# Kernel optimization log

Measured on AMD Instinct MI355X. Metric: run time of the kernel, lower is better.

The kernel has to match this reference:

```python
import jax, jax.numpy as jnp
import numpy as np

NEG = -9e15
LN_EPS = 1e-5
ALPHA = 0.2  # LeakyReLU negative slope


def setup_inputs() -> dict:
    key = jax.random.key(0)
    ks = jax.random.split(key, 10)
    B, N, Din, H, F, L = 8, 512, 64, 8, 128, 2
    x = jax.random.normal(ks[0], (B, N, Din), dtype=jnp.float32)
    adj = jax.random.randint(ks[1], (B, N, N), 0, 2, dtype=jnp.int32)
    Wp = jax.random.normal(ks[2], (Din, F), dtype=jnp.float32) * 0.12
    bp = jnp.zeros((F,), dtype=jnp.float32)
    W_heads = jax.random.normal(ks[3], (L, H, F, F), dtype=jnp.float32) * 0.08
    a_heads = jax.random.normal(ks[4], (L, H, 2 * F), dtype=jnp.float32) * 0.08
    W_out = jax.random.normal(ks[5], (L, H * F, F), dtype=jnp.float32) * 0.03
    a_out = jax.random.normal(ks[6], (L, 2 * F), dtype=jnp.float32) * 0.08
    ln_g = jnp.ones((L, F), dtype=jnp.float32)
    ln_b = jnp.zeros((L, F), dtype=jnp.float32)
    return {"x": x, "adj": adj, "Wp": Wp, "bp": bp, "W_heads": W_heads,
            "a_heads": a_heads, "W_out": W_out, "a_out": a_out,
            "ln_g": ln_g, "ln_b": ln_b}


def _gat_heads(x, W, a, adj_mask):
    # x:[B,N,Fin]  W:[H,Fin,F]  a:[H,2F]  adj_mask:[B,N,N] bool
    h = jnp.einsum('bni,hio->bhno', x, W)          # [B,H,N,F]
    F = h.shape[-1]
    # a_input @ a == (h_i . a1) + (h_j . a2): split attention vector,
    # mathematically identical to the concat formulation.
    s1 = jnp.einsum('bhnf,hf->bhn', h, a[:, :F])   # source term
    s2 = jnp.einsum('bhnf,hf->bhn', h, a[:, F:])   # target term
    e = jax.nn.leaky_relu(s1[:, :, :, None] + s2[:, :, None, :], ALPHA)  # [B,H,N,N]
    att = jnp.where(adj_mask[:, None], e, NEG)
    att = jax.nn.softmax(att, axis=-1)
    return jnp.einsum('bhnm,bhmf->bhnf', att, h)   # [B,H,N,F]


def _gat_single(x, W, a, adj_mask):
    # out_att head (concat=False, no ELU)
    h = jnp.einsum('bni,io->bno', x, W)            # [B,N,F]
    F = h.shape[-1]
    s1 = h @ a[:F]                                  # [B,N]
    s2 = h @ a[F:]
    e = jax.nn.leaky_relu(s1[:, :, None] + s2[:, None, :], ALPHA)
    att = jnp.where(adj_mask, e, NEG)
    att = jax.nn.softmax(att, axis=-1)
    return jnp.einsum('bnm,bmf->bnf', att, h)


def _layernorm(x, g, b):
    mu = jnp.mean(x, axis=-1, keepdims=True)
    var = jnp.var(x, axis=-1, keepdims=True)
    return (x - mu) * jax.lax.rsqrt(var + LN_EPS) * g + b


def reference(x, adj, Wp, bp, W_heads, a_heads, W_out, a_out, ln_g, ln_b):
    adj_mask = adj > 0                              # [B,N,N]
    L = W_heads.shape[0]
    B, N = x.shape[0], x.shape[1]
    # input projection (eval mode -> dropout is identity)
    h = jax.nn.relu(x @ Wp + bp)                    # [B,N,F]
    for i in range(L):
        residual = h
        heads = _gat_heads(h, W_heads[i], a_heads[i], adj_mask)      # [B,H,N,F]
        heads = jax.nn.elu(heads)                                     # concat=True -> ELU
        multi = jnp.transpose(heads, (0, 2, 1, 3)).reshape(B, N, -1)  # [B,N,H*F]
        out = _gat_single(multi, W_out[i], a_out[i], adj_mask)        # [B,N,F]
        h = _layernorm(out + residual, ln_g[i], ln_b[i])
        if i < L - 1:
            h = jax.nn.relu(h)
    return h
```

## Files before the change

### kernel.cpp

```cpp
#include <hip/hip_runtime.h>
#include <hip/hip_cooperative_groups.h>


namespace cg = cooperative_groups;

constexpr int B = 8, N = 512, DIN = 64, H = 8, F = 128;
constexpr int BN = B * N;
constexpr float ALPHA_LR = 0.2f;
constexpr float EPS_LN = 1e-5f;
constexpr float FLOW = -3.0e38f;

typedef __attribute__((ext_vector_type(8))) short short8;
typedef __attribute__((ext_vector_type(4))) float f32x4;

__device__ __forceinline__ f32x4 mfma16(short8 a, short8 b, f32x4 c) {
  return __builtin_amdgcn_mfma_f32_16x16x32_bf16(a, b, c, 0, 0, 0);
}

__device__ __forceinline__ short f2bf(float f) {
  union { float f; unsigned u; } v;
  v.f = f;
  unsigned r = v.u + 0x7FFFu + ((v.u >> 16) & 1u);
  return (short)(r >> 16);
}

struct KParams {
  const float* x; const int* adj; const float* Wp; const float* bp;
  const float* W_heads; const float* a_heads; const float* W_out;
  const float* a_out; const float* ln_g; const float* ln_b;
  float* h; short* hb; unsigned long long* amask; short* WTh; short* WoT;
  short* hhT; short* multi; short* hsT; float* sA; float* dout;
};

struct SM_PH { short As[64 * 136]; short Bs[128 * 136]; };
struct SM_AH {
  short Vs[128 * 136]; short Pf[16 * 64 * 8]; float s2all[512];
  float s1r[64]; float mrow[64]; float linv[64]; float red[64][4];
};
struct SM_PO { short As[32 * 136]; short Bs[32 * 136]; };
struct SM_AS {
  short Vs[128 * 136]; short Pf[4 * 64 * 8]; float s2all[512];
  float Ot[16][132]; float redS[16][16]; float redQ[16][16];
  float s1r[16]; float mrow[16]; float linv[16]; float muA[16]; float rsA[16];
};
struct SM_SU { float T[32][33]; float xr[2][64]; };

__device__ __forceinline__ void st_setup(const KParams& P, int bid, int tid,
                                         char* smraw) {
  for (int i = tid; i < 288; i += 256) P.sA[(size_t)bid * 288 + i] = 0.f;
  {
    int lane = tid & 63, wv = tid >> 6;
    int v[16];
#pragma unroll
    for (int j = 0; j < 16; j++) {
      int w = (bid + j * 512) * 4 + wv;
      v[j] = P.adj[(size_t)w * 64 + lane];
    }
#pragma unroll
    for (int j = 0; j < 16; j++) {
      int w = (bid + j * 512) * 4 + wv;
      unsigned long long m = __ballot(v[j] > 0);
      if (lane == 0) P.amask[w] = m;
    }
  }
  {
    SM_SU* s = (SM_SU*)smraw;
    int half = tid >> 7, f = tid & 127;
    for (int u = bid; u < 2048; u += 512) {
      int row = u * 2 + half;
      __syncthreads();
      if (f < 64) s->xr[half][f] = P.x[(size_t)row * DIN + f];
      __syncthreads();
      float acc = P.bp[f];
#pragma unroll
      for (int i = 0; i < DIN; i++)
        acc = fmaf(s->xr[half][i], P.Wp[i * F + f], acc);
      acc = fmaxf(acc, 0.f);
      P.h[(size_t)row * F + f] = acc;
      P.hb[(size_t)row * F + f] = f2bf(acc);
    }
  }
  {
    SM_SU* s = (SM_SU*)smraw;
    const float* in; short* out; int R, C, bx, by, bt;
    if (bid < 256) {
      in = P.W_heads; out = P.WTh; R = 128; C = 128;
      bx = bid & 3; by = (bid >> 2) & 3; bt = bid >> 4;
    } else {
      int i = bid - 256;
      in = P.W_out; out = P.WoT; R = 1024; C = 128;
      bx = i & 3; by = (i >> 2) & 31; bt = i >> 7;
    }
    int c0 = bx * 32, r0 = by * 32;
    const float* ip = in + (size_t)bt * R * C;
    short* op = out + (size_t)bt * R * C;
    __syncthreads();
    {
      int r = tid >> 3, c4 = (tid & 7) * 4;
      float4 v = *(const float4*)(ip + (size_t)(r0 + r) * C + c0 + c4);
      s->T[r][c4] = v.x; s->T[r][c4 + 1] = v.y;
      s->T[r][c4 + 2] = v.z; s->T[r][c4 + 3] = v.w;
    }
    __syncthreads();
    {
      int cr = tid >> 3, q = (tid & 7) * 4;
      short4 o;
      o.x = f2bf(s->T[q][cr]); o.y = f2bf(s->T[q + 1][cr]);
      o.z = f2bf(s->T[q + 2][cr]); o.w = f2bf(s->T[q + 3][cr]);
      *(short4*)(op + (size_t)(c0 + cr) * R + r0 + q) = o;
    }
  }
}

__device__ __forceinline__ void st_proj_heads(
    const KParams& P, const short* WT, const float* ah_base, float* s1,
    float* s2, int bid, int tid, char* smraw) {
  SM_PH* sm = (SM_PH*)smraw;
  int nt = bid & 3, ft = (bid >> 2) & 1, bh = bid >> 3;
  int b = bh >> 3, hd = bh & 7;
  int n0 = nt * 128;
  constexpr int LK = 136;
  int lane = tid & 63, w = tid >> 6;
  {
    int r = tid >> 2, q = tid & 3;
    const uint4* g = (const uint4*)(WT + ((size_t)hd * F + ft * 64 + r) * F) + q * 4;
    uint4* lp = (uint4*)(sm->As + r * LK) + q * 4;
    lp[0] = g[0]; lp[1] = g[1]; lp[2] = g[2]; lp[3] = g[3];
  }
  {
    int q = tid & 3;
    for (int r = tid >> 2; r < 128; r += 64) {
      const uint4* g = (const uint4*)(P.hb + ((size_t)(b * N + n0 + r)) * F) + q * 4;
      uint4* lp = (uint4*)(sm->Bs + r * LK) + q * 4;
      lp[0] = g[0]; lp[1] = g[1]; lp[2] = g[2]; lp[3] = g[3];
    }
  }
  __syncthreads();
  int arow = lane & 15, koff = (lane >> 4) * 8;
  f32x4 acc[4][2] = {};
#pragma unroll
  for (int ks = 0; ks < 4; ks++) {
    short8 a[4], bb[2];
#pragma unroll
    for (int rt = 0; rt < 4; rt++)
      a[rt] = *(const short8*)(sm->As + (rt * 16 + arow) * LK + ks * 32 + koff);
#pragma unroll
    for (int cj = 0; cj < 2; cj++)
      bb[cj] = *(const short8*)(sm->Bs + ((2 * w + cj) * 16 + arow) * LK +
                                ks * 32 + koff);
#pragma unroll
    for (int rt = 0; rt < 4; rt++)
#pragma unroll
      for (int cj = 0; cj < 2; cj++)
        acc[rt][cj] = mfma16(a[rt], bb[cj], acc[rt][cj]);
  }
  short* outp = P.hhT + (size_t)bh * F * N;
  int crow0 = (lane >> 4) * 4;
#pragma unroll
  for (int rt = 0; rt < 4; rt++)
#pragma unroll
    for (int cj = 0; cj < 2; cj++) {
      int fo = ft * 64 + rt * 16 + crow0;
      int n = n0 + (2 * w + cj) * 16 + arow;
#pragma unroll
      for (int r = 0; r < 4; r++)
        outp[(size_t)(fo + r) * N + n] = f2bf(acc[rt][cj][r]);
    }
  const float* ah = ah_base + (size_t)hd * 2 * F;
  float pa1[2] = {0.f, 0.f}, pa2[2] = {0.f, 0.f};
#pragma unroll
  for (int rt = 0; rt < 4; rt++) {
    int fo = ft * 64 + rt * 16 + crow0;
#pragma unroll
    for (int r = 0; r < 4; r++) {
      float a1v = ah[fo + r], a2v = ah[F + fo + r];
      pa1[0] = fmaf(a1v, acc[rt][0][r], pa1[0]);
      pa1[1] = fmaf(a1v, acc[rt][1][r], pa1[1]);
      pa2[0] = fmaf(a2v, acc[rt][0][r], pa2[0]);
      pa2[1] = fmaf(a2v, acc[rt][1][r], pa2[1]);
    }
  }
#pragma unroll
  for (int cj = 0; cj < 2; cj++) {
    float v1 = pa1[cj], v2 = pa2[cj];
    v1 += __shfl_xor(v1, 16); v1 += __shfl_xor(v1, 32);
    v2 += __shfl_xor(v2, 16); v2 += __shfl_xor(v2, 32);
    if (lane < 16) {
      int n = n0 + (2 * w + cj) * 16 + lane;
      atomicAdd(&s1[(size_t)bh * N + n], v1);
      atomicAdd(&s2[(size_t)bh * N + n], v2);
    }
  }
}

__device__ __forceinline__ void st_attn_heads(
    const KParams& P, const float* s1g, const float* s2g, int bid, int tid,
    char* smraw) {
  SM_AH* sm = (SM_AH*)smraw;
  int nt = bid & 7, hd = (bid >> 3) & 7, b = bid >> 6;
  int n0 = nt * 64, bh = b * H + hd;
  constexpr int LVK = 136;
  int lane = tid & 63, w = tid >> 6;
  sm->s2all[tid] = s2g[(size_t)bh * N + tid];
  sm->s2all[tid + 256] = s2g[(size_t)bh * N + tid + 256];
  if (tid < 64) sm->s1r[tid] = s1g[(size_t)bh * N + n0 + tid];
  __syncthreads();
  {
    const unsigned long long* mq = P.amask + ((size_t)(b * N + n0 + lane)) * 8;
    float mx = FLOW;
#pragma unroll
    for (int j = 0; j < 2; j++) {
      unsigned long long mb = mq[w * 2 + j];
      int base = w * 128 + j * 64;
      unsigned lo = (unsigned)mb, hi = (unsigned)(mb >> 32);
#pragma unroll
      for (int k = 0; k < 32; k++) {
        mx = ((lo >> k) & 1u) ? fmaxf(mx, sm->s2all[base + k]) : mx;
        mx = ((hi >> k) & 1u) ? fmaxf(mx, sm->s2all[base + 32 + k]) : mx;
      }
    }
    sm->red[lane][w] = mx;
  }
  __syncthreads();
  if (tid < 64) {
    float m2 = fmaxf(fmaxf(sm->red[tid][0], sm->red[tid][1]),
                     fmaxf(sm->red[tid][2], sm->red[tid][3]));
    float xm = sm->s1r[tid] + m2;
    sm->mrow[tid] = xm > 0.f ? xm : ALPHA_LR * xm;
  }
  float lp = 0.f;
  int arow = lane & 15, koff = (lane >> 4) * 8;
  f32x4 acc[4][2] = {};
  const short* Vg = P.hhT + (size_t)bh * F * N;
  const unsigned long long* mp = P.amask + ((size_t)(b * N + n0 + lane)) * 8;
  for (int mc = 0; mc < 4; mc++) {
    int m0 = mc * 128;
    __syncthreads();
    {
      int fr = tid >> 1, hf = tid & 1;
      const uint4* g4 = (const uint4*)(Vg + (size_t)fr * N + m0 + hf * 64);
      uint4* l4 = (uint4*)(sm->Vs + fr * LVK + hf * 64);
#pragma unroll
      for (int k = 0; k < 8; k++) l4[k] = g4[k];
    }
    {
      float s1v = sm->s1r[lane], mr = sm->mrow[lane];
      unsigned bits = (unsigned)(mp[mc * 2 + (w >> 1)] >> ((w & 1) * 32));
      short* pbase = sm->Pf + (((lane >> 4) * 4 + w) * 64) * 8;
#pragma unroll
      for (int q = 0; q < 4; q++) {
        short8 pk;
#pragma unroll
        for (int j = 0; j < 8; j++) {
          float xv = s1v + sm->s2all[m0 + w * 32 + q * 8 + j];
          xv = xv > 0.f ? xv : ALPHA_LR * xv;
          float p = __expf(xv - mr);
          p = ((bits >> (q * 8 + j)) & 1u) ? p : 0.f;
          lp += p;
          pk[j] = f2bf(p);
        }
        *(short8*)(pbase + ((q << 4) | (lane & 15)) * 8) = pk;
      }
    }
    __syncthreads();
#pragma unroll
    for (int ks = 0; ks < 4; ks++) {
      short8 a[4];
#pragma unroll
      for (int rt = 0; rt < 4; rt++)
        a[rt] = *(const short8*)(sm->Pf + ((rt * 4 + ks) * 64 + lane) * 8);
#pragma unroll
      for (int cj = 0; cj < 2; cj++) {
        short8 bb = *(const short8*)(sm->Vs + ((w * 2 + cj) * 16 + arow) * LVK +
                                     ks * 32 + koff);
#pragma unroll
        for (int rt = 0; rt < 4; rt++)
          acc[rt][cj] = mfma16(a[rt], bb, acc[rt][cj]);
      }
    }
  }
  __syncthreads();
  sm->red[lane][w] = lp;
  __syncthreads();
  if (tid < 64)
    sm->linv[tid] = 1.f / (sm->red[tid][0] + sm->red[tid][1] +
                           sm->red[tid][2] + sm->red[tid][3]);
  __syncthreads();
  int crow0 = (lane >> 4) * 4;
#pragma unroll
  for (int rt = 0; rt < 4; rt++)
#pragma unroll
    for (int cj = 0; cj < 2; cj++) {
      int fcol = (w * 2 + cj) * 16 + arow;
#pragma unroll
      for (int rr = 0; rr < 4; rr++) {
        int nrow = rt * 16 + crow0 + rr;
        float v = acc[rt][cj][rr] * sm->linv[nrow];
        v = v > 0.f ? v : __expf(v) - 1.f;
        P.multi[((size_t)(b * N + n0 + nrow)) * (H * F) + hd * F + fcol] =
            f2bf(v);
      }
    }
}

__device__ __forceinline__ void st_proj_out(
    const KParams& P, const short* WoT, const float* ao, float* s1, float* s2,
    int bid, int tid, char* smraw) {
  SM_PO* sm = (SM_PO*)smraw;
  int ft = bid & 3, nt = (bid >> 2) & 15, b = bid >> 6;
  int f0 = ft * 32, nb = nt * 32;
  constexpr int LK = 136;
  int lane = tid & 63, w = tid >> 6;
  int rt = w & 1, ct = w >> 1;
  int arow = lane & 15, koff = (lane >> 4) * 8;
  const int KT = H * F;
  f32x4 acc = {};
  for (int k0 = 0; k0 < KT; k0 += 128) {
    __syncthreads();
    {
      int r = tid >> 3, e = tid & 7;
      const uint4* gp = (const uint4*)(WoT + (size_t)(f0 + r) * KT + k0) + e * 2;
      uint4* lp = (uint4*)(sm->As + r * LK) + e * 2;
      lp[0] = gp[0]; lp[1] = gp[1];
    }
    {
      int r = tid >> 3, e = tid & 7;
      const uint4* gp =
          (const uint4*)(P.multi + (size_t)(b * N + nb + r) * KT + k0) + e * 2;
      uint4* lp = (uint4*)(sm->Bs + r * LK) + e * 2;
      lp[0] = gp[0]; lp[1] = gp[1];
    }
    __syncthreads();
#pragma unroll
    for (int ks = 0; ks < 4; ks++) {
      short8 a = *(const short8*)(sm->As + (rt * 16 + arow) * LK + ks * 32 + koff);
      short8 bb = *(const short8*)(sm->Bs + (ct * 16 + arow) * LK + ks * 32 + koff);
      acc = mfma16(a, bb, acc);
    }
  }
  int crow0 = (lane >> 4) * 4;
  short* op = P.hsT + (size_t)b * F * N;
#pragma unroll
  for (int r = 0; r < 4; r++)
    op[(size_t)(f0 + rt * 16 + crow0 + r) * N + nb + ct * 16 + arow] =
        f2bf(acc[r]);
  float pa1 = 0.f, pa2 = 0.f;
  {
    int fo = f0 + rt * 16 + crow0;
#pragma unroll
    for (int r = 0; r < 4; r++) {
      pa1 = fmaf(ao[fo + r], acc[r], pa1);
      pa2 = fmaf(ao[F + fo + r], acc[r], pa2);
    }
  }
  pa1 += __shfl_xor(pa1, 16); pa1 += __shfl_xor(pa1, 32);
  pa2 += __shfl_xor(pa2, 16); pa2 += __shfl_xor(pa2, 32);
  if (lane < 16) {
    int n = nb + ct * 16 + lane;
    atomicAdd(&s1[(size_t)b * N + n], pa1);
    atomicAdd(&s2[(size_t)b * N + n], pa2);
  }
}

__device__ __forceinline__ void st_attn_single(
    const KParams& P, const float* s1g, const float* s2g, const float* lng,
    const float* lnb, int last, int bid, int tid, char* smraw) {
  SM_AS* sm = (SM_AS*)smraw;
  int nt = bid & 31, b = bid >> 5;
  int n0 = nt * 16;
  constexpr int LVK = 136;
  int lane = tid & 63, w = tid >> 6;
  sm->s2all[tid] = s2g[(size_t)b * N + tid];
  sm->s2all[tid + 256] = s2g[(size_t)b * N + tid + 256];
  if (tid < 16) sm->s1r[tid] = s1g[(size_t)b * N + n0 + tid];
  __syncthreads();
  {
    int r = tid & 15, seg = tid >> 4;
    unsigned long long mb =
        P.amask[((size_t)(b * N + n0 + r)) * 8 + (seg >> 1)];
    unsigned bits = (unsigned)(mb >> ((seg & 1) * 32));
    float mx = FLOW;
#pragma unroll
    for (int k = 0; k < 32; k++)
      mx = ((bits >> k) & 1u) ? fmaxf(mx, sm->s2all[seg * 32 + k]) : mx;
    sm->redS[r][seg] = mx;
  }
  __syncthreads();
  if (tid < 16) {
    float m2 = FLOW;
#pragma unroll
    for (int k = 0; k < 16; k++) m2 = fmaxf(m2, sm->redS[tid][k]);
    float xm = sm->s1r[tid] + m2;
    sm->mrow[tid] = xm > 0.f ? xm : ALPHA_LR * xm;
  }
  float lp = 0.f;
  int arow = lane & 15, koff = (lane >> 4) * 8;
  int pr = tid & 15, pq = (tid >> 4) & 3;
  f32x4 acc[2] = {};
  const short* Vg = P.hsT + (size_t)b * F * N;
  const unsigned long long* mp = P.amask + ((size_t)(b * N + n0 + pr)) * 8;
  for (int mc = 0; mc < 4; mc++) {
    int m0 = mc * 128;
    __syncthreads();
    {
      int fr = tid >> 1, hf = tid & 1;
      const uint4* g4 = (const uint4*)(Vg + (size_t)fr * N + m0 + hf * 64);
      uint4* l4 = (uint4*)(sm->Vs + fr * LVK + hf * 64);
#pragma unroll
      for (int k = 0; k < 8; k++) l4[k] = g4[k];
    }
    {
      float s1v = sm->s1r[pr], mr = sm->mrow[pr];
      unsigned bits = (unsigned)(mp[mc * 2 + (w >> 1)] >> ((w & 1) * 32));
      short8 pk;
#pragma unroll
      for (int j = 0; j < 8; j++) {
        float xv = s1v + sm->s2all[m0 + w * 32 + pq * 8 + j];
        xv = xv > 0.f ? xv : ALPHA_LR * xv;
        float p = __expf(xv - mr);
        p = ((bits >> (pq * 8 + j)) & 1u) ? p : 0.f;
        lp += p;
        pk[j] = f2bf(p);
      }
      *(short8*)(sm->Pf + (w * 64 + ((pq << 4) | pr)) * 8) = pk;
    }
    __syncthreads();
#pragma unroll
    for (int ks = 0; ks < 4; ks++) {
      short8 a = *(const short8*)(sm->Pf + (ks * 64 + lane) * 8);
#pragma unroll
      for (int cj = 0; cj < 2; cj++) {
        short8 bb = *(const short8*)(sm->Vs + ((w * 2 + cj) * 16 + arow) * LVK +
                                     ks * 32 + koff);
        acc[cj] = mfma16(a, bb, acc[cj]);
      }
    }
  }
  __syncthreads();
  sm->redS[pr][tid >> 4] = lp;
  __syncthreads();
  if (tid < 16) {
    float l = 0.f;
#pragma unroll
    for (int k = 0; k < 16; k++) l += sm->redS[tid][k];
    sm->linv[tid] = 1.f / l;
  }
  __syncthreads();
  int crow0 = (lane >> 4) * 4;
#pragma unroll
  for (int cj = 0; cj < 2; cj++) {
    int fcol = (w * 2 + cj) * 16 + arow;
#pragma unroll
    for (int rr = 0; rr < 4; rr++) {
      int row = crow0 + rr;
      sm->Ot[row][fcol] = acc[cj][rr] * sm->linv[row];
    }
  }
  __syncthreads();
  int r2 = tid >> 4, f8 = (tid & 15) * 8;
  size_t gbase = ((size_t)(b * N + n0 + r2)) * F + f8;
  float v[8];
  float s = 0.f, sq = 0.f;
#pragma unroll
  for (int j = 0; j < 8; j++) {
    float t = sm->Ot[r2][f8 + j] + P.h[gbase + j];
    v[j] = t;
    s += t;
    sq = fmaf(t, t, sq);
  }
  sm->redS[r2][tid & 15] = s;
  sm->redQ[r2][tid & 15] = sq;
  __syncthreads();
  if (tid < 16) {
    float ss = 0.f, qq = 0.f;
#pragma unroll
    for (int k = 0; k < 16; k++) { ss += sm->redS[tid][k]; qq += sm->redQ[tid][k]; }
    float mu = ss * (1.f / F);
    sm->muA[tid] = mu;
    sm->rsA[tid] = rsqrtf(qq * (1.f / F) - mu * mu + EPS_LN);
  }
  __syncthreads();
  float mu = sm->muA[r2], rs = sm->rsA[r2];
#pragma unroll
  for (int j = 0; j < 8; j++) {
    float y = (v[j] - mu) * rs * lng[f8 + j] + lnb[f8 + j];
    if (last) {
      P.dout[gbase + j] = y;
    } else {
      y = fmaxf(y, 0.f);
      P.h[gbase + j] = y;
      P.hb[gbase + j] = f2bf(y);
    }
  }
}

__global__ __launch_bounds__(256, 2) void k_mega(KParams P) {
  cg::grid_group grid = cg::this_grid();
  __shared__ alignas(16) char smem[sizeof(SM_AH)];
  int bid = blockIdx.x, tid = threadIdx.x;

  st_setup(P, bid, tid, smem);
  __threadfence(); grid.sync();

  for (int l = 0; l < 2; l++) {
    const short* WTh_l = P.WTh + (size_t)l * H * F * F;
    const float* ah_l = P.a_heads + (size_t)l * H * 2 * F;
    const short* WoT_l = P.WoT + (size_t)l * H * F * F;
    const float* ao_l = P.a_out + (size_t)l * 2 * F;
    float* s1h = P.sA + (size_t)l * 73728;
    float* s2h = s1h + 32768;
    float* s1o = s2h + 32768;
    float* s2o = s1o + 4096;

    st_proj_heads(P, WTh_l, ah_l, s1h, s2h, bid, tid, smem);
    __threadfence(); grid.sync();
    st_attn_heads(P, s1h, s2h, bid, tid, smem);
    __threadfence(); grid.sync();
    st_proj_out(P, WoT_l, ao_l, s1o, s2o, bid, tid, smem);
    __threadfence(); grid.sync();
    if (bid < 256)
      st_attn_single(P, s1o, s2o, P.ln_g + (size_t)l * F,
                     P.ln_b + (size_t)l * F, l == 1, bid, tid, smem);
    if (l == 0) { __threadfence(); grid.sync(); }
  }
}

__global__ __launch_bounds__(256) void g_setup(KParams P) {
  __shared__ alignas(16) char smem[sizeof(SM_SU)];
  st_setup(P, blockIdx.x, threadIdx.x, smem);
}
__global__ __launch_bounds__(256) void g_proj_heads(KParams P, int l) {
  __shared__ alignas(16) char smem[sizeof(SM_PH)];
  float* s1h = P.sA + (size_t)l * 73728;
  st_proj_heads(P, P.WTh + (size_t)l * H * F * F,
                P.a_heads + (size_t)l * H * 2 * F, s1h, s1h + 32768,
                blockIdx.x, threadIdx.x, smem);
}
__global__ __launch_bounds__(256) void g_attn_heads(KParams P, int l) {
  __shared__ alignas(16) char smem[sizeof(SM_AH)];
  float* s1h = P.sA + (size_t)l * 73728;
  st_attn_heads(P, s1h, s1h + 32768, blockIdx.x, threadIdx.x, smem);
}
__global__ __launch_bounds__(256) void g_proj_out(KParams P, int l) {
  __shared__ alignas(16) char smem[sizeof(SM_PO)];
  float* s1o = P.sA + (size_t)l * 73728 + 65536;
  st_proj_out(P, P.WoT + (size_t)l * H * F * F,
              P.a_out + (size_t)l * 2 * F, s1o, s1o + 4096, blockIdx.x,
              threadIdx.x, smem);
}
__global__ __launch_bounds__(256) void g_attn_single(KParams P, int l) {
  __shared__ alignas(16) char smem[sizeof(SM_AS)];
  float* s1o = P.sA + (size_t)l * 73728 + 65536;
  st_attn_single(P, s1o, s1o + 4096, P.ln_g + (size_t)l * F,
                 P.ln_b + (size_t)l * F, l == 1, blockIdx.x, threadIdx.x,
                 smem);
}

extern "C" void kernel_launch(void* const* d_in, const int* in_sizes, int n_in,
                              void* d_out, int out_size, void* d_ws,
                              size_t ws_size, hipStream_t stream) {
  char* p = (char*)d_ws;
  auto alloc = [&](size_t bytes) {
    char* r = p;
    p += (bytes + 255) & ~(size_t)255;
    return r;
  };
  KParams P;
  P.x = (const float*)d_in[0];
  P.adj = (const int*)d_in[1];
  P.Wp = (const float*)d_in[2];
  P.bp = (const float*)d_in[3];
  P.W_heads = (const float*)d_in[4];
  P.a_heads = (const float*)d_in[5];
  P.W_out = (const float*)d_in[6];
  P.a_out = (const float*)d_in[7];
  P.ln_g = (const float*)d_in[8];
  P.ln_b = (const float*)d_in[9];
  P.sA = (float*)alloc((size_t)2 * 73728 * 4);
  P.WTh = (short*)alloc((size_t)2 * H * F * F * 2);
  P.WoT = (short*)alloc((size_t)2 * H * F * F * 2);
  P.amask = (unsigned long long*)alloc((size_t)BN * 8 * 8);
  P.h = (float*)alloc((size_t)BN * F * 4);
  P.hb = (short*)alloc((size_t)BN * F * 2);
  P.hhT = (short*)alloc((size_t)B * H * F * N * 2);
  P.multi = (short*)alloc((size_t)BN * H * F * 2);
  P.hsT = (short*)alloc((size_t)B * F * N * 2);
  P.dout = (float*)d_out;

  int occ = 0;
  (void)hipOccupancyMaxActiveBlocksPerMultiprocessor(&occ, k_mega, 256, 0);
  if (occ >= 2) {
    void* kargs[] = {&P};
    hipError_t e = hipLaunchCooperativeKernel((void*)k_mega, dim3(512),
                                              dim3(256), kargs, 0, stream);
    if (e == hipSuccess) return;
    (void)hipGetLastError();
  }
  g_setup<<<512, 256, 0, stream>>>(P);
  for (int l = 0; l < 2; l++) {
    g_proj_heads<<<512, 256, 0, stream>>>(P, l);
    g_attn_heads<<<512, 256, 0, stream>>>(P, l);
    g_proj_out<<<512, 256, 0, stream>>>(P, l);
    g_attn_single<<<256, 256, 0, stream>>>(P, l);
  }
}
```

Before: 195.6 us.

## Replace cooperative megakernel with separate launches, prefetch V tiles, remap block indices

Removes the cooperative persistent kernel and its grid-wide barriers, so every stage now runs as its own kernel launch with separate shared memory. The attention kernels now prefetch the next 128-column V chunk into registers while the current chunk's MFMA work runs, which should hide global-load latency. Block indices are remapped so the batch index varies fastest, spreading neighbouring blocks across different batches. The cost is nine launches instead of one, plus extra register pressure from the prefetch buffers.

```diff
diff --git a/kernel.cpp b/kernel.cpp
--- a/kernel.cpp
+++ b/kernel.cpp
@@ -1,8 +1,5 @@
 #include <hip/hip_runtime.h>
-#include <hip/hip_cooperative_groups.h>
-
-
-namespace cg = cooperative_groups;
+
 
 constexpr int B = 8, N = 512, DIN = 64, H = 8, F = 128;
 constexpr int BN = B * N;
@@ -32,21 +29,10 @@
   short* hhT; short* multi; short* hsT; float* sA; float* dout;
 };
 
-struct SM_PH { short As[64 * 136]; short Bs[128 * 136]; };
-struct SM_AH {
-  short Vs[128 * 136]; short Pf[16 * 64 * 8]; float s2all[512];
-  float s1r[64]; float mrow[64]; float linv[64]; float red[64][4];
-};
-struct SM_PO { short As[32 * 136]; short Bs[32 * 136]; };
-struct SM_AS {
-  short Vs[128 * 136]; short Pf[4 * 64 * 8]; float s2all[512];
-  float Ot[16][132]; float redS[16][16]; float redQ[16][16];
-  float s1r[16]; float mrow[16]; float linv[16]; float muA[16]; float rsA[16];
-};
-struct SM_SU { float T[32][33]; float xr[2][64]; };
-
-__device__ __forceinline__ void st_setup(const KParams& P, int bid, int tid,
-                                         char* smraw) {
+__global__ __launch_bounds__(256) void g_setup(KParams P) {
+  __shared__ float T[32][33];
+  __shared__ float xr[2][64];
+  int bid = blockIdx.x, tid = threadIdx.x;
   for (int i = tid; i < 288; i += 256) P.sA[(size_t)bid * 288 + i] = 0.f;
   {
     int lane = tid & 63, wv = tid >> 6;
@@ -64,24 +50,22 @@
     }
   }
   {
-    SM_SU* s = (SM_SU*)smraw;
     int half = tid >> 7, f = tid & 127;
     for (int u = bid; u < 2048; u += 512) {
       int row = u * 2 + half;
       __syncthreads();
-      if (f < 64) s->xr[half][f] = P.x[(size_t)row * DIN + f];
+      if (f < 64) xr[half][f] = P.x[(size_t)row * DIN + f];
       __syncthreads();
       float acc = P.bp[f];
 #pragma unroll
       for (int i = 0; i < DIN; i++)
-        acc = fmaf(s->xr[half][i], P.Wp[i * F + f], acc);
+        acc = fmaf(xr[half][i], P.Wp[i * F + f], acc);
       acc = fmaxf(acc, 0.f);
       P.h[(size_t)row * F + f] = acc;
       P.hb[(size_t)row * F + f] = f2bf(acc);
     }
   }
   {
-    SM_SU* s = (SM_SU*)smraw;
     const float* in; short* out; int R, C, bx, by, bt;
     if (bid < 256) {
       in = P.W_heads; out = P.WTh; R = 128; C = 128;
@@ -98,40 +82,43 @@
     {
       int r = tid >> 3, c4 = (tid & 7) * 4;
       float4 v = *(const float4*)(ip + (size_t)(r0 + r) * C + c0 + c4);
-      s->T[r][c4] = v.x; s->T[r][c4 + 1] = v.y;
-      s->T[r][c4 + 2] = v.z; s->T[r][c4 + 3] = v.w;
+      T[r][c4] = v.x; T[r][c4 + 1] = v.y; T[r][c4 + 2] = v.z; T[r][c4 + 3] = v.w;
     }
     __syncthreads();
     {
       int cr = tid >> 3, q = (tid & 7) * 4;
       short4 o;
-      o.x = f2bf(s->T[q][cr]); o.y = f2bf(s->T[q + 1][cr]);
-      o.z = f2bf(s->T[q + 2][cr]); o.w = f2bf(s->T[q + 3][cr]);
+      o.x = f2bf(T[q][cr]); o.y = f2bf(T[q + 1][cr]);
+      o.z = f2bf(T[q + 2][cr]); o.w = f2bf(T[q + 3][cr]);
       *(short4*)(op + (size_t)(c0 + cr) * R + r0 + q) = o;
     }
   }
 }
 
-__device__ __forceinline__ void st_proj_heads(
-    const KParams& P, const short* WT, const float* ah_base, float* s1,
-    float* s2, int bid, int tid, char* smraw) {
-  SM_PH* sm = (SM_PH*)smraw;
-  int nt = bid & 3, ft = (bid >> 2) & 1, bh = bid >> 3;
-  int b = bh >> 3, hd = bh & 7;
-  int n0 = nt * 128;
+__global__ __launch_bounds__(256) void g_proj_heads(KParams P, int l) {
   constexpr int LK = 136;
+  __shared__ short As[64 * LK];
+  __shared__ short Bs[128 * LK];
+  const short* WT = P.WTh + (size_t)l * H * F * F;
+  const float* ah_base = P.a_heads + (size_t)l * H * 2 * F;
+  float* s1 = P.sA + (size_t)l * 73728;
+  float* s2 = s1 + 32768;
+  int bid = blockIdx.x, tid = threadIdx.x;
+  int b = bid & 7, u = bid >> 3;
+  int hd = u & 7, ft = (u >> 3) & 1, nt = u >> 4;
+  int bh = b * 8 + hd, n0 = nt * 128;
   int lane = tid & 63, w = tid >> 6;
   {
     int r = tid >> 2, q = tid & 3;
     const uint4* g = (const uint4*)(WT + ((size_t)hd * F + ft * 64 + r) * F) + q * 4;
-    uint4* lp = (uint4*)(sm->As + r * LK) + q * 4;
+    uint4* lp = (uint4*)(As + r * LK) + q * 4;
     lp[0] = g[0]; lp[1] = g[1]; lp[2] = g[2]; lp[3] = g[3];
   }
   {
     int q = tid & 3;
     for (int r = tid >> 2; r < 128; r += 64) {
       const uint4* g = (const uint4*)(P.hb + ((size_t)(b * N + n0 + r)) * F) + q * 4;
-      uint4* lp = (uint4*)(sm->Bs + r * LK) + q * 4;
+      uint4* lp = (uint4*)(Bs + r * LK) + q * 4;
       lp[0] = g[0]; lp[1] = g[1]; lp[2] = g[2]; lp[3] = g[3];
     }
   }
@@ -143,11 +130,10 @@
     short8 a[4], bb[2];
 #pragma unroll
     for (int rt = 0; rt < 4; rt++)
-      a[rt] = *(const short8*)(sm->As + (rt * 16 + arow) * LK + ks * 32 + koff);
+      a[rt] = *(const short8*)(As + (rt * 16 + arow) * LK + ks * 32 + koff);
 #pragma unroll
     for (int cj = 0; cj < 2; cj++)
-      bb[cj] = *(const short8*)(sm->Bs + ((2 * w + cj) * 16 + arow) * LK +
-                                ks * 32 + koff);
+      bb[cj] = *(const short8*)(Bs + ((2 * w + cj) * 16 + arow) * LK + ks * 32 + koff);
 #pragma unroll
     for (int rt = 0; rt < 4; rt++)
 #pragma unroll
@@ -193,17 +179,31 @@
   }
 }
 
-__device__ __forceinline__ void st_attn_heads(
-    const KParams& P, const float* s1g, const float* s2g, int bid, int tid,
-    char* smraw) {
-  SM_AH* sm = (SM_AH*)smraw;
-  int nt = bid & 7, hd = (bid >> 3) & 7, b = bid >> 6;
-  int n0 = nt * 64, bh = b * H + hd;
+__global__ __launch_bounds__(256) void g_attn_heads(KParams P, int l) {
   constexpr int LVK = 136;
+  __shared__ short Vs[128 * LVK];
+  __shared__ short Pf[16 * 64 * 8];
+  __shared__ float s2all[512];
+  __shared__ float s1r[64], mrow[64], linv[64];
+  __shared__ float red[64][4];
+  const float* s1g = P.sA + (size_t)l * 73728;
+  const float* s2g = s1g + 32768;
+  int bid = blockIdx.x, tid = threadIdx.x;
+  int bh = bid & 63, nt = bid >> 6;
+  int b = bh >> 3, n0 = nt * 64;
   int lane = tid & 63, w = tid >> 6;
-  sm->s2all[tid] = s2g[(size_t)bh * N + tid];
-  sm->s2all[tid + 256] = s2g[(size_t)bh * N + tid + 256];
-  if (tid < 64) sm->s1r[tid] = s1g[(size_t)bh * N + n0 + tid];
+  sm_pre:;
+  s2all[tid] = s2g[(size_t)bh * N + tid];
+  s2all[tid + 256] = s2g[(size_t)bh * N + tid + 256];
+  if (tid < 64) s1r[tid] = s1g[(size_t)bh * N + n0 + tid];
+  const short* Vg = P.hhT + (size_t)bh * F * N;
+  int fr = tid >> 1, hf = tid & 1;
+  uint4 vreg[8];
+  {
+    const uint4* g4 = (const uint4*)(Vg + (size_t)fr * N + 0 + hf * 64);
+#pragma unroll
+    for (int k = 0; k < 8; k++) vreg[k] = g4[k];
+  }
   __syncthreads();
   {
     const unsigned long long* mq = P.amask + ((size_t)(b * N + n0 + lane)) * 8;
@@ -215,44 +215,41 @@
       unsigned lo = (unsigned)mb, hi = (unsigned)(mb >> 32);
 #pragma unroll
       for (int k = 0; k < 32; k++) {
-        mx = ((lo >> k) & 1u) ? fmaxf(mx, sm->s2all[base + k]) : mx;
-        mx = ((hi >> k) & 1u) ? fmaxf(mx, sm->s2all[base + 32 + k]) : mx;
+        mx = ((lo >> k) & 1u) ? fmaxf(mx, s2all[base + k]) : mx;
+        mx = ((hi >> k) & 1u) ? fmaxf(mx, s2all[base + 32 + k]) : mx;
       }
     }
-    sm->red[lane][w] = mx;
+    red[lane][w] = mx;
   }
   __syncthreads();
   if (tid < 64) {
-    float m2 = fmaxf(fmaxf(sm->red[tid][0], sm->red[tid][1]),
-                     fmaxf(sm->red[tid][2], sm->red[tid][3]));
-    float xm = sm->s1r[tid] + m2;
-    sm->mrow[tid] = xm > 0.f ? xm : ALPHA_LR * xm;
+    float m2 = fmaxf(fmaxf(red[tid][0], red[tid][1]),
+                     fmaxf(red[tid][2], red[tid][3]));
+    float xm = s1r[tid] + m2;
+    mrow[tid] = xm > 0.f ? xm : ALPHA_LR * xm;
   }
   float lp = 0.f;
   int arow = lane & 15, koff = (lane >> 4) * 8;
   f32x4 acc[4][2] = {};
-  const short* Vg = P.hhT + (size_t)bh * F * N;
   const unsigned long long* mp = P.amask + ((size_t)(b * N + n0 + lane)) * 8;
   for (int mc = 0; mc < 4; mc++) {
     int m0 = mc * 128;
     __syncthreads();
     {
-      int fr = tid >> 1, hf = tid & 1;
-      const uint4* g4 = (const uint4*)(Vg + (size_t)fr * N + m0 + hf * 64);
-      uint4* l4 = (uint4*)(sm->Vs + fr * LVK + hf * 64);
-#pragma unroll
-      for (int k = 0; k < 8; k++) l4[k] = g4[k];
-    }
-    {
-      float s1v = sm->s1r[lane], mr = sm->mrow[lane];
+      uint4* l4 = (uint4*)(Vs + fr * LVK + hf * 64);
+#pragma unroll
+      for (int k = 0; k < 8; k++) l4[k] = vreg[k];
+    }
+    {
+      float s1v = s1r[lane], mr = mrow[lane];
       unsigned bits = (unsigned)(mp[mc * 2 + (w >> 1)] >> ((w & 1) * 32));
-      short* pbase = sm->Pf + (((lane >> 4) * 4 + w) * 64) * 8;
+      short* pbase = Pf + (((lane >> 4) * 4 + w) * 64) * 8;
 #pragma unroll
       for (int q = 0; q < 4; q++) {
         short8 pk;
 #pragma unroll
         for (int j = 0; j < 8; j++) {
-          float xv = s1v + sm->s2all[m0 + w * 32 + q * 8 + j];
+          float xv = s1v + s2all[m0 + w * 32 + q * 8 + j];
           xv = xv > 0.f ? xv : ALPHA_LR * xv;
           float p = __expf(xv - mr);
           p = ((bits >> (q * 8 + j)) & 1u) ? p : 0.f;
@@ -263,15 +260,20 @@
       }
     }
     __syncthreads();
+    if (mc < 3) {
+      const uint4* g4 = (const uint4*)(Vg + (size_t)fr * N + (m0 + 128) + hf * 64);
+#pragma unroll
+      for (int k = 0; k < 8; k++) vreg[k] = g4[k];
+    }
 #pragma unroll
     for (int ks = 0; ks < 4; ks++) {
       short8 a[4];
 #pragma unroll
       for (int rt = 0; rt < 4; rt++)
-        a[rt] = *(const short8*)(sm->Pf + ((rt * 4 + ks) * 64 + lane) * 8);
+        a[rt] = *(const short8*)(Pf + ((rt * 4 + ks) * 64 + lane) * 8);
 #pragma unroll
       for (int cj = 0; cj < 2; cj++) {
-        short8 bb = *(const short8*)(sm->Vs + ((w * 2 + cj) * 16 + arow) * LVK +
+        short8 bb = *(const short8*)(Vs + ((w * 2 + cj) * 16 + arow) * LVK +
                                      ks * 32 + koff);
 #pragma unroll
         for (int rt = 0; rt < 4; rt++)
@@ -280,13 +282,13 @@
     }
   }
   __syncthreads();
-  sm->red[lane][w] = lp;
+  red[lane][w] = lp;
   __syncthreads();
   if (tid < 64)
-    sm->linv[tid] = 1.f / (sm->red[tid][0] + sm->red[tid][1] +
-                           sm->red[tid][2] + sm->red[tid][3]);
+    linv[tid] = 1.f / (red[tid][0] + red[tid][1] + red[tid][2] + red[tid][3]);
   __syncthreads();
   int crow0 = (lane >> 4) * 4;
+  int hd = bh & 7;
 #pragma unroll
   for (int rt = 0; rt < 4; rt++)
 #pragma unroll
@@ -295,7 +297,7 @@
 #pragma unroll
       for (int rr = 0; rr < 4; rr++) {
         int nrow = rt * 16 + crow0 + rr;
-        float v = acc[rt][cj][rr] * sm->linv[nrow];
+        float v = acc[rt][cj][rr] * linv[nrow];
         v = v > 0.f ? v : __expf(v) - 1.f;
         P.multi[((size_t)(b * N + n0 + nrow)) * (H * F) + hd * F + fcol] =
             f2bf(v);
@@ -303,13 +305,17 @@
     }
 }
 
-__device__ __forceinline__ void st_proj_out(
-    const KParams& P, const short* WoT, const float* ao, float* s1, float* s2,
-    int bid, int tid, char* smraw) {
-  SM_PO* sm = (SM_PO*)smraw;
-  int ft = bid & 3, nt = (bid >> 2) & 15, b = bid >> 6;
+__global__ __launch_bounds__(256) void g_proj_out(KParams P, int l) {
+  constexpr int LK = 136;
+  __shared__ short As[32 * LK];
+  __shared__ short Bs[32 * LK];
+  const short* WoT = P.WoT + (size_t)l * H * F * F;
+  const float* ao = P.a_out + (size_t)l * 2 * F;
+  float* s1 = P.sA + (size_t)l * 73728 + 65536;
+  float* s2 = s1 + 4096;
+  int bid = blockIdx.x, tid = threadIdx.x;
+  int b = bid & 7, nt = (bid >> 3) & 15, ft = bid >> 7;
   int f0 = ft * 32, nb = nt * 32;
-  constexpr int LK = 136;
   int lane = tid & 63, w = tid >> 6;
   int rt = w & 1, ct = w >> 1;
   int arow = lane & 15, koff = (lane >> 4) * 8;
@@ -320,21 +326,21 @@
     {
       int r = tid >> 3, e = tid & 7;
       const uint4* gp = (const uint4*)(WoT + (size_t)(f0 + r) * KT + k0) + e * 2;
-      uint4* lp = (uint4*)(sm->As + r * LK) + e * 2;
+      uint4* lp = (uint4*)(As + r * LK) + e * 2;
       lp[0] = gp[0]; lp[1] = gp[1];
     }
     {
       int r = tid >> 3, e = tid & 7;
       const uint4* gp =
           (const uint4*)(P.multi + (size_t)(b * N + nb + r) * KT + k0) + e * 2;
-      uint4* lp = (uint4*)(sm->Bs + r * LK) + e * 2;
+      uint4* lp = (uint4*)(Bs + r * LK) + e * 2;
       lp[0] = gp[0]; lp[1] = gp[1];
     }
     __syncthreads();
 #pragma unroll
     for (int ks = 0; ks < 4; ks++) {
-      short8 a = *(const short8*)(sm->As + (rt * 16 + arow) * LK + ks * 32 + koff);
-      short8 bb = *(const short8*)(sm->Bs + (ct * 16 + arow) * LK + ks * 32 + koff);
+      short8 a = *(const short8*)(As + (rt * 16 + arow) * LK + ks * 32 + koff);
+      short8 bb = *(const short8*)(Bs + (ct * 16 + arow) * LK + ks * 32 + koff);
       acc = mfma16(a, bb, acc);
     }
   }
@@ -362,88 +368,106 @@
   }
 }
 
-__device__ __forceinline__ void st_attn_single(
-    const KParams& P, const float* s1g, const float* s2g, const float* lng,
-    const float* lnb, int last, int bid, int tid, char* smraw) {
-  SM_AS* sm = (SM_AS*)smraw;
-  int nt = bid & 31, b = bid >> 5;
+__global__ __launch_bounds__(256) void g_attn_single(KParams P, int l) {
+  constexpr int LVK = 136;
+  __shared__ short Vs[128 * LVK];
+  __shared__ short Pf[4 * 64 * 8];
+  __shared__ float s2all[512];
+  __shared__ float Ot[16][132];
+  __shared__ float redS[16][16], redQ[16][16];
+  __shared__ float s1r[16], mrow[16], linv[16], muA[16], rsA[16];
+  const float* s1g = P.sA + (size_t)l * 73728 + 65536;
+  const float* s2g = s1g + 4096;
+  const float* lng = P.ln_g + (size_t)l * F;
+  const float* lnb = P.ln_b + (size_t)l * F;
+  int last = l == 1;
+  int bid = blockIdx.x, tid = threadIdx.x;
+  int b = bid & 7, nt = bid >> 3;
   int n0 = nt * 16;
-  constexpr int LVK = 136;
   int lane = tid & 63, w = tid >> 6;
-  sm->s2all[tid] = s2g[(size_t)b * N + tid];
-  sm->s2all[tid + 256] = s2g[(size_t)b * N + tid + 256];
-  if (tid < 16) sm->s1r[tid] = s1g[(size_t)b * N + n0 + tid];
+  s2all[tid] = s2g[(size_t)b * N + tid];
+  s2all[tid + 256] = s2g[(size_t)b * N + tid + 256];
+  if (tid < 16) s1r[tid] = s1g[(size_t)b * N + n0 + tid];
+  const short* Vg = P.hsT + (size_t)b * F * N;
+  int fr = tid >> 1, hf = tid & 1;
+  uint4 vreg[8];
+  {
+    const uint4* g4 = (const uint4*)(Vg + (size_t)fr * N + 0 + hf * 64);
+#pragma unroll
+    for (int k = 0; k < 8; k++) vreg[k] = g4[k];
+  }
   __syncthreads();
   {
     int r = tid & 15, seg = tid >> 4;
-    unsigned long long mb =
-        P.amask[((size_t)(b * N + n0 + r)) * 8 + (seg >> 1)];
+    unsigned long long mb = P.amask[((size_t)(b * N + n0 + r)) * 8 + (seg >> 1)];
     unsigned bits = (unsigned)(mb >> ((seg & 1) * 32));
     float mx = FLOW;
 #pragma unroll
     for (int k = 0; k < 32; k++)
-      mx = ((bits >> k) & 1u) ? fmaxf(mx, sm->s2all[seg * 32 + k]) : mx;
-    sm->redS[r][seg] = mx;
+      mx = ((bits >> k) & 1u) ? fmaxf(mx, s2all[seg * 32 + k]) : mx;
+    redS[r][seg] = mx;
   }
   __syncthreads();
   if (tid < 16) {
     float m2 = FLOW;
 #pragma unroll
-    for (int k = 0; k < 16; k++) m2 = fmaxf(m2, sm->redS[tid][k]);
-    float xm = sm->s1r[tid] + m2;
-    sm->mrow[tid] = xm > 0.f ? xm : ALPHA_LR * xm;
+    for (int k = 0; k < 16; k++) m2 = fmaxf(m2, redS[tid][k]);
+    float xm = s1r[tid] + m2;
+    mrow[tid] = xm > 0.f ? xm : ALPHA_LR * xm;
   }
   float lp = 0.f;
   int arow = lane & 15, koff = (lane >> 4) * 8;
   int pr = tid & 15, pq = (tid >> 4) & 3;
   f32x4 acc[2] = {};
-  const short* Vg = P.hsT + (size_t)b * F * N;
   const unsigned long long* mp = P.amask + ((size_t)(b * N + n0 + pr)) * 8;
   for (int mc = 0; mc < 4; mc++) {
     int m0 = mc * 128;
     __syncthreads();
     {
-      int fr = tid >> 1, hf = tid & 1;
-      const uint4* g4 = (const uint4*)(Vg + (size_t)fr * N + m0 + hf * 64);
-      uint4* l4 = (uint4*)(sm->Vs + fr * LVK + hf * 64);
-#pragma unroll
-      for (int k = 0; k < 8; k++) l4[k] = g4[k];
-    }
-    {
-      float s1v = sm->s1r[pr], mr = sm->mrow[pr];
+      uint4* l4 = (uint4*)(Vs + fr * LVK + hf * 64);
+#pragma unroll
+      for (int k = 0; k < 8; k++) l4[k] = vreg[k];
+    }
+    {
+      float s1v = s1r[pr], mr = mrow[pr];
       unsigned bits = (unsigned)(mp[mc * 2 + (w >> 1)] >> ((w & 1) * 32));
       short8 pk;
 #pragma unroll
       for (int j = 0; j < 8; j++) {
-        float xv = s1v + sm->s2all[m0 + w * 32 + pq * 8 + j];
+        float xv = s1v + s2all[m0 + w * 32 + pq * 8 + j];
         xv = xv > 0.f ? xv : ALPHA_LR * xv;
         float p = __expf(xv - mr);
         p = ((bits >> (pq * 8 + j)) & 1u) ? p : 0.f;
         lp += p;
         pk[j] = f2bf(p);
       }
-      *(short8*)(sm->Pf + (w * 64 + ((pq << 4) | pr)) * 8) = pk;
-    }
-    __syncthreads();
+      *(short8*)(Pf + (w * 64 + ((pq << 4) | pr)) * 8) = pk;
+    }
+    __syncthreads();
+    if (mc < 3) {
+      const uint4* g4 = (const uint4*)(Vg + (size_t)fr * N + (m0 + 128) + hf * 64);
+#pragma unroll
+      for (int k = 0; k < 8; k++) vreg[k] = g4[k];
+    }
 #pragma unroll
     for (int ks = 0; ks < 4; ks++) {
-      short8 a = *(const short8*)(sm->Pf + (ks * 64 + lane) * 8);
+      short8 a = *(const short8*)(Pf + (ks * 64 + lane) * 8);
 #pragma unroll
       for (int cj = 0; cj < 2; cj++) {
-        short8 bb = *(const short8*)(sm->Vs + ((w * 2 + cj) * 16 + arow) * LVK +
+        short8 bb = *(const short8*)(Vs + ((w * 2 + cj) * 16 + arow) * LVK +
                                      ks * 32 + koff);
         acc[cj] = mfma16(a, bb, acc[cj]);
       }
     }
   }
   __syncthreads();
-  sm->redS[pr][tid >> 4] = lp;
+  redS[pr][tid >> 4] = lp;
   __syncthreads();
   if (tid < 16) {
-    float l = 0.f;
-#pragma unroll
-    for (int k = 0; k < 16; k++) l += sm->redS[tid][k];
-    sm->linv[tid] = 1.f / l;
+    float lsum = 0.f;
+#pragma unroll
+    for (int k = 0; k < 16; k++) lsum += redS[tid][k];
+    linv[tid] = 1.f / lsum;
   }
   __syncthreads();
   int crow0 = (lane >> 4) * 4;
@@ -453,7 +477,7 @@
 #pragma unroll
     for (int rr = 0; rr < 4; rr++) {
       int row = crow0 + rr;
-      sm->Ot[row][fcol] = acc[cj][rr] * sm->linv[row];
+      Ot[row][fcol] = acc[cj][rr] * linv[row];
     }
   }
   __syncthreads();
@@ -463,24 +487,24 @@
   float s = 0.f, sq = 0.f;
 #pragma unroll
   for (int j = 0; j < 8; j++) {
-    float t = sm->Ot[r2][f8 + j] + P.h[gbase + j];
+    float t = Ot[r2][f8 + j] + P.h[gbase + j];
     v[j] = t;
     s += t;
     sq = fmaf(t, t, sq);
   }
-  sm->redS[r2][tid & 15] = s;
-  sm->redQ[r2][tid & 15] = sq;
+  redS[r2][tid & 15] = s;
+  redQ[r2][tid & 15] = sq;
   __syncthreads();
   if (tid < 16) {
     float ss = 0.f, qq = 0.f;
 #pragma unroll
-    for (int k = 0; k < 16; k++) { ss += sm->redS[tid][k]; qq += sm->redQ[tid][k]; }
+    for (int k = 0; k < 16; k++) { ss += redS[tid][k]; qq += redQ[tid][k]; }
     float mu = ss * (1.f / F);
-    sm->muA[tid] = mu;
-    sm->rsA[tid] = rsqrtf(qq * (1.f / F) - mu * mu + EPS_LN);
-  }
-  __syncthreads();
-  float mu = sm->muA[r2], rs = sm->rsA[r2];
+    muA[tid] = mu;
+    rsA[tid] = rsqrtf(qq * (1.f / F) - mu * mu + EPS_LN);
+  }
+  __syncthreads();
+  float mu = muA[r2], rs = rsA[r2];
 #pragma unroll
   for (int j = 0; j < 8; j++) {
     float y = (v[j] - mu) * rs * lng[f8 + j] + lnb[f8 + j];
@@ -492,68 +516,6 @@
       P.hb[gbase + j] = f2bf(y);
     }
   }
-}
-
-__global__ __launch_bounds__(256, 2) void k_mega(KParams P) {
-  cg::grid_group grid = cg::this_grid();
-  __shared__ alignas(16) char smem[sizeof(SM_AH)];
-  int bid = blockIdx.x, tid = threadIdx.x;
-
-  st_setup(P, bid, tid, smem);
-  __threadfence(); grid.sync();
-
-  for (int l = 0; l < 2; l++) {
-    const short* WTh_l = P.WTh + (size_t)l * H * F * F;
-    const float* ah_l = P.a_heads + (size_t)l * H * 2 * F;
-    const short* WoT_l = P.WoT + (size_t)l * H * F * F;
-    const float* ao_l = P.a_out + (size_t)l * 2 * F;
-    float* s1h = P.sA + (size_t)l * 73728;
-    float* s2h = s1h + 32768;
-    float* s1o = s2h + 32768;
-    float* s2o = s1o + 4096;
-
-    st_proj_heads(P, WTh_l, ah_l, s1h, s2h, bid, tid, smem);
-    __threadfence(); grid.sync();
-    st_attn_heads(P, s1h, s2h, bid, tid, smem);
-    __threadfence(); grid.sync();
-    st_proj_out(P, WoT_l, ao_l, s1o, s2o, bid, tid, smem);
-    __threadfence(); grid.sync();
-    if (bid < 256)
-      st_attn_single(P, s1o, s2o, P.ln_g + (size_t)l * F,
-                     P.ln_b + (size_t)l * F, l == 1, bid, tid, smem);
-    if (l == 0) { __threadfence(); grid.sync(); }
-  }
-}
-
-__global__ __launch_bounds__(256) void g_setup(KParams P) {
-  __shared__ alignas(16) char smem[sizeof(SM_SU)];
-  st_setup(P, blockIdx.x, threadIdx.x, smem);
-}
-__global__ __launch_bounds__(256) void g_proj_heads(KParams P, int l) {
-  __shared__ alignas(16) char smem[sizeof(SM_PH)];
-  float* s1h = P.sA + (size_t)l * 73728;
-  st_proj_heads(P, P.WTh + (size_t)l * H * F * F,
-                P.a_heads + (size_t)l * H * 2 * F, s1h, s1h + 32768,
-                blockIdx.x, threadIdx.x, smem);
-}
-__global__ __launch_bounds__(256) void g_attn_heads(KParams P, int l) {
-  __shared__ alignas(16) char smem[sizeof(SM_AH)];
-  float* s1h = P.sA + (size_t)l * 73728;
-  st_attn_heads(P, s1h, s1h + 32768, blockIdx.x, threadIdx.x, smem);
-}
-__global__ __launch_bounds__(256) void g_proj_out(KParams P, int l) {
-  __shared__ alignas(16) char smem[sizeof(SM_PO)];
-  float* s1o = P.sA + (size_t)l * 73728 + 65536;
-  st_proj_out(P, P.WoT + (size_t)l * H * F * F,
-              P.a_out + (size_t)l * 2 * F, s1o, s1o + 4096, blockIdx.x,
-              threadIdx.x, smem);
-}
-__global__ __launch_bounds__(256) void g_attn_single(KParams P, int l) {
-  __shared__ alignas(16) char smem[sizeof(SM_AS)];
-  float* s1o = P.sA + (size_t)l * 73728 + 65536;
-  st_attn_single(P, s1o, s1o + 4096, P.ln_g + (size_t)l * F,
-                 P.ln_b + (size_t)l * F, l == 1, blockIdx.x, threadIdx.x,
-                 smem);
 }
 
 extern "C" void kernel_launch(void* const* d_in, const int* in_sizes, int n_in,
@@ -587,15 +549,6 @@
   P.hsT = (short*)alloc((size_t)B * F * N * 2);
   P.dout = (float*)d_out;
 
-  int occ = 0;
-  (void)hipOccupancyMaxActiveBlocksPerMultiprocessor(&occ, k_mega, 256, 0);
-  if (occ >= 2) {
-    void* kargs[] = {&P};
-    hipError_t e = hipLaunchCooperativeKernel((void*)k_mega, dim3(512),
-                                              dim3(256), kargs, 0, stream);
-    if (e == hipSuccess) return;
-    (void)hipGetLastError();
-  }
   g_setup<<<512, 256, 0, stream>>>(P);
   for (int l = 0; l < 2; l++) {
     g_proj_heads<<<512, 256, 0, stream>>>(P, l);
```

After: 233.3 us. 19.3% more time.
